# Kernel optimization log

Measured on AMD Instinct MI355X. Metric: run time of the kernel, lower is better.

## Reference

```python
import jax, jax.numpy as jnp
import numpy as np

EPS = 1e-6
DIM_HEAD = 32
INP = 128
OUP = 128
IH = IW = 32


def _conv3x3(x, w):
    # NCHW conv, 3x3, stride 1, pad 1, no bias
    return jax.lax.conv_general_dilated(
        x, w, window_strides=(1, 1), padding=((1, 1), (1, 1)),
        dimension_numbers=("NCHW", "OIHW", "NCHW"))


def _groupnorm1(x, gamma, beta):
    # GroupNorm with 1 group: normalize over (C,H,W) per sample
    m = jnp.mean(x, axis=(1, 2, 3), keepdims=True)
    v = jnp.var(x, axis=(1, 2, 3), keepdims=True)
    xn = (x - m) * jax.lax.rsqrt(v + EPS)
    return xn * gamma[None, :, None, None] + beta[None, :, None, None]


def _proj(x, w, gamma, beta):
    return jax.nn.gelu(_groupnorm1(_conv3x3(x, w), gamma, beta), approximate=False)


def _relative_index(ih, iw):
    coords = np.stack(np.meshgrid(np.arange(ih), np.arange(iw), indexing="ij"))
    coords = coords.reshape(2, -1)  # (2, N)
    rel = coords[:, :, None] - coords[:, None, :]  # (2, N, N)
    rel[0] += ih - 1
    rel[1] += iw - 1
    rel[0] *= 2 * iw - 1
    return rel.sum(0).reshape(-1).astype(np.int32)  # (N*N,)


def setup_inputs() -> dict:
    key = jax.random.key(0)
    ks = jax.random.split(key, 12)
    B = 16
    x = jax.random.normal(ks[0], (B, INP, IH, IW), jnp.float32)
    w_scale = 0.05
    wq = jax.random.normal(ks[1], (INP, INP, 3, 3), jnp.float32) * w_scale
    wk = jax.random.normal(ks[2], (INP, INP, 3, 3), jnp.float32) * w_scale
    wv = jax.random.normal(ks[3], (INP, INP, 3, 3), jnp.float32) * w_scale
    gq = jnp.ones((INP,), jnp.float32); bq = jnp.zeros((INP,), jnp.float32)
    gk = jnp.ones((INP,), jnp.float32); bk = jnp.zeros((INP,), jnp.float32)
    gv = jnp.ones((INP,), jnp.float32); bv = jnp.zeros((INP,), jnp.float32)
    heads = INP // DIM_HEAD
    table = jax.random.normal(ks[4], ((2 * IH - 1) * (2 * IW - 1), heads), jnp.float32) * 0.02
    rel_index = jnp.asarray(_relative_index(IH, IW))
    out_w = jax.random.normal(ks[5], (OUP, INP, 1, 1), jnp.float32) * w_scale
    out_b = jnp.zeros((OUP,), jnp.float32)
    return {"x": x, "wq": wq, "gq": gq, "bq": bq, "wk": wk, "gk": gk, "bk": bk,
            "wv": wv, "gv": gv, "bv": bv, "table": table, "rel_index": rel_index,
            "out_w": out_w, "out_b": out_b}


def reference(x, wq, gq, bq, wk, gk, bk, wv, gv, bv, table, rel_index, out_w, out_b):
    B, C, ih, iw = x.shape
    H = C // DIM_HEAD
    N = ih * iw

    def to_heads(t):
        # b c ih iw -> b (ihiw) c -> b h n d (heads-major channel split)
        return t.reshape(B, C, N).transpose(0, 2, 1).reshape(B, N, H, DIM_HEAD).transpose(0, 2, 1, 3)

    q = to_heads(_proj(x, wq, gq, bq))
    k = to_heads(_proj(x, wk, gk, bk))
    v = to_heads(_proj(x, wv, gv, bv))

    # NOTE: original applies self.scale only when y is not None; y=None here -> no scale
    dots = jnp.einsum("bhnd,bhmd->bhnm", q, k)  # (B,H,N,N)

    bias = table[rel_index]                 # (N*N, H)
    bias = bias.reshape(N, N, H).transpose(2, 0, 1)[None]  # (1,H,N,N)
    attn = jax.nn.softmax(dots + bias, axis=-1)

    out = jnp.einsum("bhnm,bhmd->bhnd", attn, v)
    out = out.transpose(0, 2, 1, 3).reshape(B, N, C).transpose(0, 2, 1).reshape(B, C, ih, iw)
    # to_out: 1x1 conv + bias (Dropout2d is identity in eval)
    out = jax.lax.conv_general_dilated(
        out, out_w, window_strides=(1, 1), padding=((0, 0), (0, 0)),
        dimension_numbers=("NCHW", "OIHW", "NCHW")) + out_b[None, :, None, None]
    return out
```

## Files before the change

### kernel.cpp

```cpp
#include <hip/hip_runtime.h>

typedef unsigned short u16;
typedef unsigned int   u32;

#define NB   16
#define NC   128
#define NPIX 1024
#define NH   4
#define DH   32

typedef __attribute__((ext_vector_type(8))) short short8;
typedef __attribute__((ext_vector_type(4))) float f32x4;
typedef __attribute__((ext_vector_type(8))) _Float16 half8;

#define XROWS 1152

__device__ __forceinline__ float bf2f(u16 u) {
    return __uint_as_float(((u32)u) << 16);
}
__device__ __forceinline__ u16 f2bf(float f) {
    u32 u = __float_as_uint(f);
    u32 r = (u + 0x7fffu + ((u >> 16) & 1u)) >> 16;
    return (u16)r;
}
__device__ __forceinline__ u16 f2h(float f) {
    _Float16 h = (_Float16)f;
    u16 r; __builtin_memcpy(&r, &h, 2); return r;
}
__device__ __forceinline__ int pk_h2(float a, float b) {
    auto h = __builtin_amdgcn_cvt_pkrtz(a, b);
    int r; __builtin_memcpy(&r, &h, 4); return r;
}
__device__ __forceinline__ float loadf(const void* p, int i, int isf) {
    return isf ? ((const float*)p)[i] : bf2f(((const u16*)p)[i]);
}
__device__ __forceinline__ float4 load4(const void* p, int i4, int isf) {
    if (isf) return ((const float4*)p)[i4];
    ushort4 u = ((const ushort4*)p)[i4];
    return make_float4(bf2f(u.x), bf2f(u.y), bf2f(u.z), bf2f(u.w));
}
__device__ __forceinline__ int detect_isf(const void* x) {
    const u16* p = (const u16*)x;
    u16 v = p[threadIdx.x & 63];
    int e = (v >> 7) & 0xFF;
    unsigned long long m = __ballot(e >= 134);
    return m != 0ull ? 1 : 0;
}

__global__ __launch_bounds__(256) void prep_all(
        const void* __restrict__ x,
        const void* __restrict__ w0, const void* __restrict__ w1,
        const void* __restrict__ w2, const void* __restrict__ ow,
        const int* __restrict__ rel, const void* __restrict__ table,
        u16* __restrict__ Wt, u16* __restrict__ Wf, u16* __restrict__ xTp,
        u16* __restrict__ biasT, float* __restrict__ stats) {
    __shared__ __align__(16) u32 smem_u[4160];
    int isf = detect_isf(x);
    int bid = blockIdx.x;
    int t = threadIdx.x;

    if (bid < 1792) {
        if (bid == 0 && t < 96) stats[t] = 0.f;
        int i = bid * 256 + t;
        if (i < 442368) {
            int j   = i / 147456;
            int rr  = i % 147456;
            int tap = rr >> 14;
            int co  = (rr >> 7) & 127;
            int ci  = rr & 127;
            const void* w = (j == 0) ? w0 : ((j == 1) ? w1 : w2);
            float v = loadf(w, (co * 128 + ci) * 9 + tap, isf);
            Wt[i] = f2bf(v);
        } else {
            int i2 = i - 442368;
            if (i2 < 16384) Wf[i2] = f2h(loadf(ow, i2, isf));
        }
    } else if (bid < 2304) {
        float* tile = (float*)smem_u;
        int b2 = bid - 1792;
        int pixg = b2 & 7, cig = (b2 >> 3) & 3, b = b2 >> 5;

        if (pixg == 0 || pixg == 7) {
            int row = (pixg == 0 ? 0 : 1088) + (t >> 2);
            int seg = t & 3;
            size_t dst = ((size_t)(b * XROWS + row)) * 128 + cig * 32 + seg * 8;
            *(uint4*)&xTp[dst] = make_uint4(0, 0, 0, 0);
        }

        int ci = t >> 3, px0 = (t & 7) * 16;
        int base = b * (NC * NPIX) + (cig * 32 + ci) * NPIX + pixg * 128 + px0;
#pragma unroll
        for (int u = 0; u < 4; ++u) {
            float4 v = load4(x, (base >> 2) + u, isf);
            float* d = &tile[ci * 129 + px0 + u * 4];
            d[0] = v.x; d[1] = v.y; d[2] = v.z; d[3] = v.w;
        }
        __syncthreads();
#pragma unroll
        for (int u = 0; u < 2; ++u) {
            int c = t + u * 256;
            int pix = c >> 2, seg = c & 3;
            u16 tmp[8];
#pragma unroll
            for (int e = 0; e < 8; ++e)
                tmp[e] = f2bf(tile[(seg * 8 + e) * 129 + pix]);
            size_t dst = ((size_t)(b * XROWS + 64 + pixg * 128 + pix)) * 128
                       + cig * 32 + seg * 8;
            *(ushort4*)&xTp[dst] =
                make_ushort4(tmp[0], tmp[1], tmp[2], tmp[3]);
            *(ushort4*)&xTp[dst + 4] =
                make_ushort4(tmp[4], tmp[5], tmp[6], tmp[7]);
        }
    } else {
        int* rl = (int*)smem_u;
        int b2 = bid - 2304;
        int nt = b2 & 15, mt = b2 >> 4;

#pragma unroll
        for (int c = 0; c < 16; ++c) {
            int i = t + c * 256;
            int r = i >> 6, cc = i & 63;
            rl[r * 65 + cc] = rel[(size_t)(nt * 64 + r) * 1024 + mt * 64 + cc];
        }
        __syncthreads();

#pragma unroll
        for (int h = 0; h < NH; ++h) {
#pragma unroll
            for (int c = 0; c < 16; ++c) {
                int wdx = t + c * 256;
                int m = wdx >> 6, n = wdx & 63;
                int ri = rl[n * 65 + m];
                float v = loadf(table, ri * NH + h, isf);
                biasT[((size_t)h << 20) + (size_t)(mt * 64 + m) * 1024
                      + nt * 64 + n] = f2bf(v);
            }
        }
    }
}

__global__ __launch_bounds__(256) void conv6_kernel(
        const u16* __restrict__ xTp, const u16* __restrict__ Wt,
        float* __restrict__ conv_out, float* __restrict__ stats) {
    __shared__ __align__(16) u16 Xh[194 * 128];

    int t = threadIdx.x;
    int bx = blockIdx.x, b = blockIdx.y, j = blockIdx.z;
    int pt = bx >> 1, coh = bx & 1;
    int p0 = pt * 128;
    int w = t >> 6, lane = t & 63;
    int q = lane >> 4, l16 = lane & 15;
    int cobase = coh * 64 + (w & 1) * 32;
    int pixbase = (w >> 1) * 64;

    const u16* xb  = xTp + ((size_t)b * XROWS + 64) * 128;
    const u16* wjb = Wt + (size_t)j * 9 * 16384;

    const u16* wr0 = wjb + (size_t)(cobase + 0 * 16 + l16) * 128 + q * 8;
    const u16* wr1 = wjb + (size_t)(cobase + 1 * 16 + l16) * 128 + q * 8;

    short8 awA[2][4], awB[2][4];
#pragma unroll
    for (int ks = 0; ks < 4; ++ks) {
        awA[0][ks] = *(const short8*)(wr0 + ks * 32);
        awA[1][ks] = *(const short8*)(wr1 + ks * 32);
    }

#pragma unroll
    for (int k = 0; k < 13; ++k) {
        int c = t + k * 256;
        if (c < 194 * 16) {
            int row = c >> 4, seg = c & 15;
            int pg = p0 - 33 + row;
            uint4 v = *(const uint4*)(xb + (size_t)pg * 128 + seg * 8);
            *(uint4*)&Xh[row * 128 + ((seg + row) & 15) * 8] = v;
        }
    }
    __syncthreads();

    f32x4 acc[2][4];
#pragma unroll
    for (int mt = 0; mt < 2; ++mt)
#pragma unroll
        for (int nt = 0; nt < 4; ++nt) acc[mt][nt] = (f32x4)0.f;

#pragma unroll
    for (int tap = 0; tap < 9; ++tap) {
        const int dy = tap / 3, dx = tap % 3;
        bool inv_e = (dx == 0) && (l16 == 0);
        bool inv_o = (dx == 2) && (l16 == 15);
        int rbase = pixbase + dy * 32 + dx + l16;

        if (tap < 8) {
            const u16* nw0 = wr0 + (size_t)(tap + 1) * 16384;
            const u16* nw1 = wr1 + (size_t)(tap + 1) * 16384;
            if ((tap & 1) == 0) {
#pragma unroll
                for (int ks = 0; ks < 4; ++ks) {
                    awB[0][ks] = *(const short8*)(nw0 + ks * 32);
                    awB[1][ks] = *(const short8*)(nw1 + ks * 32);
                }
            } else {
#pragma unroll
                for (int ks = 0; ks < 4; ++ks) {
                    awA[0][ks] = *(const short8*)(nw0 + ks * 32);
                    awA[1][ks] = *(const short8*)(nw1 + ks * 32);
                }
            }
        }

#pragma unroll
        for (int ks = 0; ks < 4; ++ks) {
            int sl = ks * 4 + q;
            short8 bf[4];
#pragma unroll
            for (int nt = 0; nt < 4; ++nt) {
                int row = rbase + nt * 16;
                short8 v = *(const short8*)&Xh[row * 128
                                               + ((sl + row) & 15) * 8];
                bf[nt] = ((nt & 1) ? inv_o : inv_e) ? (short8)0 : v;
            }
#pragma unroll
            for (int mt = 0; mt < 2; ++mt) {
                short8 a = ((tap & 1) == 0) ? awA[mt][ks] : awB[mt][ks];
#pragma unroll
                for (int nt = 0; nt < 4; ++nt)
                    acc[mt][nt] = __builtin_amdgcn_mfma_f32_16x16x32_bf16(
                        a, bf[nt], acc[mt][nt], 0, 0, 0);
            }
        }
    }

    float s = 0.f, s2 = 0.f;
    size_t obase = ((size_t)(j * NB + b) * NC) * NPIX;
#pragma unroll
    for (int mt = 0; mt < 2; ++mt) {
#pragma unroll
        for (int nt = 0; nt < 4; ++nt) {
            f32x4 v = acc[mt][nt];
            int co  = cobase + mt * 16 + q * 4;
            int pix = p0 + pixbase + nt * 16 + l16;
#pragma unroll
            for (int r = 0; r < 4; ++r) {
                float val = v[r];
                conv_out[obase + (size_t)(co + r) * NPIX + pix] = val;
                s += val;
                s2 = fmaf(val, val, s2);
            }
        }
    }
#pragma unroll
    for (int off = 32; off; off >>= 1) {
        s  += __shfl_down(s,  (unsigned)off, 64);
        s2 += __shfl_down(s2, (unsigned)off, 64);
    }
    if (lane == 0) {
        atomicAdd(&stats[(j * NB + b) * 2 + 0], s);
        atomicAdd(&stats[(j * NB + b) * 2 + 1], s2);
    }
}

__global__ __launch_bounds__(256) void norm_kernel(
        const void* __restrict__ xdet,
        const float* __restrict__ conv_out, const float* __restrict__ stats,
        const void* __restrict__ g0, const void* __restrict__ b0,
        const void* __restrict__ g1, const void* __restrict__ b1,
        const void* __restrict__ g2, const void* __restrict__ b2,
        u16* __restrict__ qh, u16* __restrict__ kh, u16* __restrict__ vh) {
    __shared__ float tile[32 * 257];
    int isf = detect_isf(xdet);
    int t = threadIdx.x;
    int n0 = blockIdx.x * 256;
    int h = blockIdx.y;
    int z = blockIdx.z;
    int j = z >> 4;
    int b = z & 15;
    const void* gam = (j == 0) ? g0 : ((j == 1) ? g1 : g2);
    const void* bet = (j == 0) ? b0 : ((j == 1) ? b1 : b2);

    float sum = stats[z * 2], ss = stats[z * 2 + 1];
    const float inv = 1.0f / 131072.0f;
    float mean = sum * inv;
    float var  = fmaxf(ss * inv - mean * mean, 0.f);
    float rstd = rsqrtf(var + 1e-6f);

    const float* src = conv_out + ((size_t)z * NC + h * DH) * NPIX + n0;

    if (j == 2) {
        u16* dst = vh + (((size_t)(b * NH + h)) * DH) * NPIX + n0;
#pragma unroll
        for (int cl = 0; cl < 32; ++cl) {
            float v = src[cl * NPIX + t];
            v = (v - mean) * rstd * loadf(gam, h * DH + cl, isf)
              + loadf(bet, h * DH + cl, isf);
            v = 0.5f * v * (1.0f + erff(v * 0.70710678118654752f));
            dst[(size_t)cl * NPIX + t] = f2h(v);
        }
        return;
    }

#pragma unroll
    for (int cl = 0; cl < 32; ++cl) tile[cl * 257 + t] = src[cl * NPIX + t];
    __syncthreads();

    u16* dst = ((j == 0) ? qh : kh)
             + (((size_t)(b * NH + h)) * NPIX + n0) * DH;
#pragma unroll
    for (int k = 0; k < 32; ++k) {
        int o = t + k * 256;
        int d = o & 31, nl = o >> 5;
        float v = tile[d * 257 + nl];
        v = (v - mean) * rstd * loadf(gam, h * DH + d, isf)
          + loadf(bet, h * DH + d, isf);
        v = 0.5f * v * (1.0f + erff(v * 0.70710678118654752f));
        dst[o] = f2h(v);
    }
}

__global__ __launch_bounds__(256) void attn2_kernel(
        const u16* __restrict__ qh, const u16* __restrict__ kh,
        const u16* __restrict__ vh, const u16* __restrict__ biasT,
        u16* __restrict__ attfh) {
    int t = threadIdx.x;
    int b = blockIdx.x, h = blockIdx.y, qt = blockIdx.z;
    int w = t >> 6, lane = t & 63, q = lane >> 4, l16 = lane & 15;
    int nrow0 = qt * 128 + w * 32;

    const u16* qb = qh + (((size_t)(b * NH + h)) * NPIX) * DH;
    const u16* kb = kh + (((size_t)(b * NH + h)) * NPIX) * DH;
    const u16* vb = vh + (((size_t)(b * NH + h)) * DH) * NPIX;
    const u16* bb = biasT + ((size_t)h << 20);

    half8 qf[2];
#pragma unroll
    for (int nt = 0; nt < 2; ++nt)
        qf[nt] = *(const half8*)(qb + (size_t)(nrow0 + nt * 16 + l16) * DH
                                 + q * 8);

    f32x4 O[2][2];
#pragma unroll
    for (int dt = 0; dt < 2; ++dt)
#pragma unroll
        for (int nt = 0; nt < 2; ++nt) O[dt][nt] = (f32x4)0.f;
    float mrow[2] = {-1e30f, -1e30f}, lrow[2] = {0.f, 0.f};

    int addrLo = ((2 * (q & 1)) * 16 + l16) * 4;
    int addrHi = addrLo + 64;
    bool hiQ = (q >= 2);

    for (int kc = 0; kc < 8; ++kc) {
        int m0 = kc * 128;
        f32x4 St[8][2];
#pragma unroll
        for (int mt = 0; mt < 8; ++mt) {
            half8 kf = *(const half8*)(kb + (size_t)(m0 + mt * 16 + l16) * DH
                                       + q * 8);
            St[mt][0] = __builtin_amdgcn_mfma_f32_16x16x32_f16(
                kf, qf[0], (f32x4)0.f, 0, 0, 0);
            St[mt][1] = __builtin_amdgcn_mfma_f32_16x16x32_f16(
                kf, qf[1], (f32x4)0.f, 0, 0, 0);
        }
        float mx[2] = {-1e30f, -1e30f};
#pragma unroll
        for (int mt = 0; mt < 8; ++mt)
#pragma unroll
            for (int nt = 0; nt < 2; ++nt) {
                const u16* bp = bb + (size_t)(m0 + mt * 16 + q * 4) * 1024
                              + nrow0 + nt * 16 + l16;
#pragma unroll
                for (int r = 0; r < 4; ++r) {
                    float v = St[mt][nt][r] + bf2f(bp[(size_t)r * 1024]);
                    St[mt][nt][r] = v;
                    mx[nt] = fmaxf(mx[nt], v);
                }
            }
        float alpha[2];
#pragma unroll
        for (int nt = 0; nt < 2; ++nt) {
            mx[nt] = fmaxf(mx[nt], __shfl_xor(mx[nt], 16, 64));
            mx[nt] = fmaxf(mx[nt], __shfl_xor(mx[nt], 32, 64));
            float mn = fmaxf(mrow[nt], mx[nt]);
            alpha[nt] = __expf(mrow[nt] - mn);
            mrow[nt] = mn;
        }
        float sm[2] = {0.f, 0.f};
#pragma unroll
        for (int mt = 0; mt < 8; ++mt)
#pragma unroll
            for (int nt = 0; nt < 2; ++nt)
#pragma unroll
                for (int r = 0; r < 4; ++r) {
                    float p = __expf(St[mt][nt][r] - mrow[nt]);
                    St[mt][nt][r] = p;
                    sm[nt] += p;
                }
#pragma unroll
        for (int nt = 0; nt < 2; ++nt) {
            sm[nt] += __shfl_xor(sm[nt], 16, 64);
            sm[nt] += __shfl_xor(sm[nt], 32, 64);
            lrow[nt] = lrow[nt] * alpha[nt] + sm[nt];
        }
#pragma unroll
        for (int dt = 0; dt < 2; ++dt)
#pragma unroll
            for (int nt = 0; nt < 2; ++nt)
#pragma unroll
                for (int r = 0; r < 4; ++r)
                    O[dt][nt][r] *= alpha[nt];
#pragma unroll
        for (int ms = 0; ms < 4; ++ms) {
            half8 vf[2];
#pragma unroll
            for (int dt = 0; dt < 2; ++dt)
                vf[dt] = *(const half8*)(vb + (size_t)(dt * 16 + l16) * NPIX
                                         + m0 + ms * 32 + q * 8);
#pragma unroll
            for (int nt = 0; nt < 2; ++nt) {
                int p01_0 = pk_h2(St[2 * ms][nt][0],     St[2 * ms][nt][1]);
                int p23_0 = pk_h2(St[2 * ms][nt][2],     St[2 * ms][nt][3]);
                int p01_1 = pk_h2(St[2 * ms + 1][nt][0], St[2 * ms + 1][nt][1]);
                int p23_1 = pk_h2(St[2 * ms + 1][nt][2], St[2 * ms + 1][nt][3]);
                int a0 = __builtin_amdgcn_ds_bpermute(addrLo, p01_0);
                int a1 = __builtin_amdgcn_ds_bpermute(addrLo, p23_0);
                int a2 = __builtin_amdgcn_ds_bpermute(addrHi, p01_0);
                int a3 = __builtin_amdgcn_ds_bpermute(addrHi, p23_0);
                int b0 = __builtin_amdgcn_ds_bpermute(addrLo, p01_1);
                int b1 = __builtin_amdgcn_ds_bpermute(addrLo, p23_1);
                int b2 = __builtin_amdgcn_ds_bpermute(addrHi, p01_1);
                int b3 = __builtin_amdgcn_ds_bpermute(addrHi, p23_1);
                int pb[4];
                pb[0] = hiQ ? b0 : a0;
                pb[1] = hiQ ? b1 : a1;
                pb[2] = hiQ ? b2 : a2;
                pb[3] = hiQ ? b3 : a3;
                half8 pf; __builtin_memcpy(&pf, pb, 16);
#pragma unroll
                for (int dt = 0; dt < 2; ++dt)
                    O[dt][nt] = __builtin_amdgcn_mfma_f32_16x16x32_f16(
                        vf[dt], pf, O[dt][nt], 0, 0, 0);
            }
        }
    }

#pragma unroll
    for (int nt = 0; nt < 2; ++nt) {
        float rl = 1.0f / lrow[nt];
        int n = nrow0 + nt * 16 + l16;
        u16* dst = attfh + ((size_t)b * NPIX + n) * NC + h * DH;
#pragma unroll
        for (int dt = 0; dt < 2; ++dt) {
            f32x4 o = O[dt][nt];
            uint2 pv = make_uint2((u32)pk_h2(o[0] * rl, o[1] * rl),
                                  (u32)pk_h2(o[2] * rl, o[3] * rl));
            *(uint2*)(dst + dt * 16 + q * 4) = pv;
        }
    }
}

__global__ __launch_bounds__(256) void out3_kernel(
        const void* __restrict__ xdet,
        const u16* __restrict__ attfh, const u16* __restrict__ Wf,
        const void* __restrict__ ob, void* __restrict__ out) {
    int isf = detect_isf(xdet);
    int t = threadIdx.x;
    int n0 = blockIdx.x * 64, b = blockIdx.y;
    int w = t >> 6, lane = t & 63, q = lane >> 4, l16 = lane & 15;
    int cobase = (w & 1) * 64, nbase = (w >> 1) * 32;

    f32x4 acc[4][2];
#pragma unroll
    for (int mt = 0; mt < 4; ++mt)
#pragma unroll
        for (int nt = 0; nt < 2; ++nt) acc[mt][nt] = (f32x4)0.f;

    const u16* ab = attfh + ((size_t)b * NPIX + n0 + nbase) * NC;
#pragma unroll
    for (int ks = 0; ks < 4; ++ks) {
        int k0 = ks * 32 + q * 8;
        half8 a[4], bfr[2];
#pragma unroll
        for (int mt = 0; mt < 4; ++mt)
            a[mt] = *(const half8*)(Wf + (size_t)(cobase + mt * 16 + l16) * NC
                                    + k0);
#pragma unroll
        for (int nt = 0; nt < 2; ++nt)
            bfr[nt] = *(const half8*)(ab + (size_t)(nt * 16 + l16) * NC + k0);
#pragma unroll
        for (int mt = 0; mt < 4; ++mt)
#pragma unroll
            for (int nt = 0; nt < 2; ++nt)
                acc[mt][nt] = __builtin_amdgcn_mfma_f32_16x16x32_f16(
                    a[mt], bfr[nt], acc[mt][nt], 0, 0, 0);
    }

#pragma unroll
    for (int mt = 0; mt < 4; ++mt) {
#pragma unroll
        for (int nt = 0; nt < 2; ++nt) {
            f32x4 v = acc[mt][nt];
            int n = n0 + nbase + nt * 16 + l16;
#pragma unroll
            for (int r = 0; r < 4; ++r) {
                int co = cobase + mt * 16 + q * 4 + r;
                float val = v[r] + loadf(ob, co, isf);
                size_t oidx = ((size_t)b * NC + co) * NPIX + n;
                if (isf) ((float*)out)[oidx] = val;
                else     ((u16*)out)[oidx]   = f2bf(val);
            }
        }
    }
}

extern "C" void kernel_launch(void* const* d_in, const int* in_sizes, int n_in,
                              void* d_out, int out_size, void* d_ws,
                              size_t ws_size, hipStream_t stream) {
    (void)in_sizes; (void)n_in; (void)out_size; (void)ws_size;
    const void* x     = d_in[0];
    const void* wq    = d_in[1];
    const void* gq    = d_in[2];
    const void* bq    = d_in[3];
    const void* wk    = d_in[4];
    const void* gk    = d_in[5];
    const void* bk    = d_in[6];
    const void* wv    = d_in[7];
    const void* gv    = d_in[8];
    const void* bv    = d_in[9];
    const void* table = d_in[10];
    const int*  rel   = (const int*)d_in[11];
    const void* ow    = d_in[12];
    const void* ob    = d_in[13];

    char* ws = (char*)d_ws;
    float* stats = (float*)(ws);
    char*  regQ  = ws + 512;
    u16*   xTp   = (u16*)regQ;
    u16*   Wt    = (u16*)(regQ + 5242880);
    u16*   qhp   = (u16*)regQ;
    u16*   khp   = (u16*)(regQ + 4194304);
    u16*   vhp   = (u16*)(regQ + 8388608);
    u16*   biasT = (u16*)(regQ + 12582912);
    u16*   Wf    = (u16*)(regQ + 20971520);
    char*  regA  = regQ + 25165824;
    float* conv  = (float*)regA;
    u16*   attfh = (u16*)(regA + 8388608);

    prep_all<<<2560, 256, 0, stream>>>(x, wq, wk, wv, ow, rel, table,
                                       Wt, Wf, xTp, biasT, stats);
    conv6_kernel<<<dim3(16, 16, 3), 256, 0, stream>>>(xTp, Wt, conv, stats);
    norm_kernel<<<dim3(4, 4, 48), 256, 0, stream>>>(x, conv, stats,
                                                    gq, bq, gk, bk, gv, bv,
                                                    qhp, khp, vhp);
    attn2_kernel<<<dim3(16, 4, 8), 256, 0, stream>>>(qhp, khp, vhp, biasT,
                                                     attfh);
    out3_kernel<<<dim3(16, 16), 256, 0, stream>>>(x, attfh, Wf, ob, d_out);
}
```

Before: 218.5 us.

## Transpose bias layout, fold bias into MFMA accumulator, split out-proj grid

The precomputed relative-position bias is now stored query-major, so each lane reads four contiguous bf16 values with one vector load instead of four strided scalar loads. Those values seed the MFMA accumulator, which removes the separate bias-add pass before the row max. Separately, the output 1x1 conv kernel splits its output channels over a new grid z dimension, doubling the block count and halving per-block accumulators. The trade-off is more redundant activation loads in the projection kernel and a different write pattern in the prep kernel.

Result: slower. 240.5 us (+10.1%).

```diff
diff --git a/kernel.cpp b/kernel.cpp
--- a/kernel.cpp
+++ b/kernel.cpp
@@ -129,11 +129,11 @@
 #pragma unroll
             for (int c = 0; c < 16; ++c) {
                 int wdx = t + c * 256;
-                int m = wdx >> 6, n = wdx & 63;
+                int m = wdx & 63, n = wdx >> 6;
                 int ri = rl[n * 65 + m];
                 float v = loadf(table, ri * NH + h, isf);
-                biasT[((size_t)h << 20) + (size_t)(mt * 64 + m) * 1024
-                      + nt * 64 + n] = f2bf(v);
+                biasT[((size_t)h << 20) + (size_t)(nt * 64 + n) * 1024
+                      + mt * 64 + m] = f2bf(v);
             }
         }
     }
@@ -330,6 +330,8 @@
     const u16* kb = kh + (((size_t)(b * NH + h)) * NPIX) * DH;
     const u16* vb = vh + (((size_t)(b * NH + h)) * DH) * NPIX;
     const u16* bb = biasT + ((size_t)h << 20);
+    const u16* bbn0 = bb + (size_t)(nrow0 + 0 * 16 + l16) * 1024 + q * 4;
+    const u16* bbn1 = bb + (size_t)(nrow0 + 1 * 16 + l16) * 1024 + q * 4;
 
     half8 qf[2];
 #pragma unroll
@@ -355,25 +357,26 @@
         for (int mt = 0; mt < 8; ++mt) {
             half8 kf = *(const half8*)(kb + (size_t)(m0 + mt * 16 + l16) * DH
                                        + q * 8);
+            ushort4 bv0 = *(const ushort4*)(bbn0 + m0 + mt * 16);
+            ushort4 bv1 = *(const ushort4*)(bbn1 + m0 + mt * 16);
+            f32x4 c0, c1;
+            c0[0] = bf2f(bv0.x); c0[1] = bf2f(bv0.y);
+            c0[2] = bf2f(bv0.z); c0[3] = bf2f(bv0.w);
+            c1[0] = bf2f(bv1.x); c1[1] = bf2f(bv1.y);
+            c1[2] = bf2f(bv1.z); c1[3] = bf2f(bv1.w);
             St[mt][0] = __builtin_amdgcn_mfma_f32_16x16x32_f16(
-                kf, qf[0], (f32x4)0.f, 0, 0, 0);
+                kf, qf[0], c0, 0, 0, 0);
             St[mt][1] = __builtin_amdgcn_mfma_f32_16x16x32_f16(
-                kf, qf[1], (f32x4)0.f, 0, 0, 0);
+                kf, qf[1], c1, 0, 0, 0);
         }
         float mx[2] = {-1e30f, -1e30f};
 #pragma unroll
         for (int mt = 0; mt < 8; ++mt)
 #pragma unroll
-            for (int nt = 0; nt < 2; ++nt) {
-                const u16* bp = bb + (size_t)(m0 + mt * 16 + q * 4) * 1024
-                              + nrow0 + nt * 16 + l16;
-#pragma unroll
-                for (int r = 0; r < 4; ++r) {
-                    float v = St[mt][nt][r] + bf2f(bp[(size_t)r * 1024]);
-                    St[mt][nt][r] = v;
-                    mx[nt] = fmaxf(mx[nt], v);
-                }
-            }
+            for (int nt = 0; nt < 2; ++nt)
+#pragma unroll
+                for (int r = 0; r < 4; ++r)
+                    mx[nt] = fmaxf(mx[nt], St[mt][nt][r]);
         float alpha[2];
 #pragma unroll
         for (int nt = 0; nt < 2; ++nt) {
@@ -463,13 +466,13 @@
         const void* __restrict__ ob, void* __restrict__ out) {
     int isf = detect_isf(xdet);
     int t = threadIdx.x;
-    int n0 = blockIdx.x * 64, b = blockIdx.y;
+    int n0 = blockIdx.x * 64, b = blockIdx.y, zc = blockIdx.z;
     int w = t >> 6, lane = t & 63, q = lane >> 4, l16 = lane & 15;
-    int cobase = (w & 1) * 64, nbase = (w >> 1) * 32;
-
-    f32x4 acc[4][2];
-#pragma unroll
-    for (int mt = 0; mt < 4; ++mt)
+    int cobase = zc * 64 + (w & 1) * 32, nbase = (w >> 1) * 32;
+
+    f32x4 acc[2][2];
+#pragma unroll
+    for (int mt = 0; mt < 2; ++mt)
 #pragma unroll
         for (int nt = 0; nt < 2; ++nt) acc[mt][nt] = (f32x4)0.f;
 
@@ -477,16 +480,16 @@
 #pragma unroll
     for (int ks = 0; ks < 4; ++ks) {
         int k0 = ks * 32 + q * 8;
-        half8 a[4], bfr[2];
-#pragma unroll
-        for (int mt = 0; mt < 4; ++mt)
+        half8 a[2], bfr[2];
+#pragma unroll
+        for (int mt = 0; mt < 2; ++mt)
             a[mt] = *(const half8*)(Wf + (size_t)(cobase + mt * 16 + l16) * NC
                                     + k0);
 #pragma unroll
         for (int nt = 0; nt < 2; ++nt)
             bfr[nt] = *(const half8*)(ab + (size_t)(nt * 16 + l16) * NC + k0);
 #pragma unroll
-        for (int mt = 0; mt < 4; ++mt)
+        for (int mt = 0; mt < 2; ++mt)
 #pragma unroll
             for (int nt = 0; nt < 2; ++nt)
                 acc[mt][nt] = __builtin_amdgcn_mfma_f32_16x16x32_f16(
@@ -494,7 +497,7 @@
     }
 
 #pragma unroll
-    for (int mt = 0; mt < 4; ++mt) {
+    for (int mt = 0; mt < 2; ++mt) {
 #pragma unroll
         for (int nt = 0; nt < 2; ++nt) {
             f32x4 v = acc[mt][nt];
@@ -552,5 +555,5 @@
                                                     qhp, khp, vhp);
     attn2_kernel<<<dim3(16, 4, 8), 256, 0, stream>>>(qhp, khp, vhp, biasT,
                                                      attfh);
-    out3_kernel<<<dim3(16, 16), 256, 0, stream>>>(x, attfh, Wf, ob, d_out);
-}
+    out3_kernel<<<dim3(16, 16, 2), 256, 0, stream>>>(x, attfh, Wf, ob, d_out);
+}
```
